# Kernel tuning notes

Measured on AMD Instinct MI355X. Metric: run time of the kernel, lower is better.

Reference implementation:

```python
import jax, jax.numpy as jnp
from jax import lax
import numpy as np

N_LAYERS = 2
HIDDEN = 1024
N_STOCKS = 1024
LB, UB = 0.0, 0.2
REBAL_ITERS = 32  # fixed upper bound; loop converges in 1-2 iters in practice


def setup_inputs() -> dict:
    key = jax.random.key(0)
    ks = jax.random.split(key, 20)
    B, T = 512, 128
    inp = {"x": jax.random.normal(ks[0], (B, T, N_STOCKS), dtype=jnp.float32)}
    k = 1
    for l in range(N_LAYERS):
        in_dim = N_STOCKS if l == 0 else HIDDEN
        s = 1.0 / np.sqrt(HIDDEN)
        inp[f"w_ih_{l}"] = jax.random.uniform(ks[k], (3 * HIDDEN, in_dim), minval=-s, maxval=s); k += 1
        inp[f"w_hh_{l}"] = jax.random.uniform(ks[k], (3 * HIDDEN, HIDDEN), minval=-s, maxval=s); k += 1
        inp[f"b_ih_{l}"] = jax.random.uniform(ks[k], (3 * HIDDEN,), minval=-s, maxval=s); k += 1
        inp[f"b_hh_{l}"] = jax.random.uniform(ks[k], (3 * HIDDEN,), minval=-s, maxval=s); k += 1
    s = 1.0 / np.sqrt(HIDDEN)
    inp["fc_w"] = jax.random.uniform(ks[k], (N_STOCKS, HIDDEN), minval=-s, maxval=s); k += 1
    inp["fc_b"] = jax.random.uniform(ks[k], (N_STOCKS,), minval=-s, maxval=s)
    return inp


def _gru_layer(x, w_ih, w_hh, b_ih, b_hh):
    # x: [B,T,D] -> hidden sequence [B,T,H]; PyTorch GRU cell math
    B, T, _ = x.shape
    H = w_hh.shape[1]
    x_proj = jnp.einsum('btd,gd->btg', x, w_ih) + b_ih  # [B,T,3H]

    def step(h, xp):
        hp = h @ w_hh.T + b_hh
        xr, xz, xn = jnp.split(xp, 3, axis=-1)
        hr, hz, hn = jnp.split(hp, 3, axis=-1)
        r = jax.nn.sigmoid(xr + hr)
        z = jax.nn.sigmoid(xz + hz)
        n = jnp.tanh(xn + r * hn)
        h_new = (1.0 - z) * n + z * h
        return h_new, h_new

    h0 = jnp.zeros((B, H), x.dtype)
    _, hs = lax.scan(step, h0, jnp.swapaxes(x_proj, 0, 1))  # [T,B,H]
    return jnp.swapaxes(hs, 0, 1)


def _rebalance(w, lb, ub, n_iters=REBAL_ITERS):
    # Batched version of the iterative capped-simplex redistribution loop.
    old = w
    wc = jnp.clip(w, lb, ub)
    done = jnp.zeros((w.shape[0],), dtype=bool)

    def body(state, _):
        old, wc, done = state
        leftover = jnp.sum(old - wc, axis=-1, keepdims=True)            # [B,1]
        mask = wc != ub                                                  # nominees
        num = jnp.sum(mask, axis=-1)                                     # [B]
        nom_sum = jnp.sum(jnp.where(mask, wc, 0.0), axis=-1, keepdims=True)
        gift = leftover * wc / jnp.where(nom_sum == 0.0, 1.0, nom_sum)
        wc_new = jnp.where(mask, wc + gift, wc)
        no_nom = num == 0
        over = jnp.any(wc_new > ub, axis=-1)
        new_done = done | no_nom | (~over)
        wc_next = jnp.where(no_nom[:, None], wc,
                            jnp.where(over[:, None], jnp.clip(wc_new, lb, ub), wc_new))
        old_next = jnp.where(no_nom[:, None], old, wc_new)
        wc_out = jnp.where(done[:, None], wc, wc_next)
        old_out = jnp.where(done[:, None], old, old_next)
        return (old_out, wc_out, new_done), None

    (_, wc, _), _ = lax.scan(body, (old, wc, done), None, length=n_iters)
    return wc


def reference(x, w_ih_0, w_hh_0, b_ih_0, b_hh_0, w_ih_1, w_hh_1, b_ih_1, b_hh_1, fc_w, fc_b):
    h = _gru_layer(x, w_ih_0, w_hh_0, b_ih_0, b_hh_0)
    h = _gru_layer(h, w_ih_1, w_hh_1, b_ih_1, b_hh_1)
    h_t = h[:, -1, :]                                   # last time step [B,H]
    logit = h_t @ fc_w.T + fc_b                         # dropout is identity in eval
    logit = jax.nn.silu(logit)
    probs = jax.nn.softmax(logit, axis=-1)
    return _rebalance(probs, LB, UB)
```

## Files before the change

### kernel.cpp

```cpp
#include <hip/hip_runtime.h>
#include <hip/hip_bf16.h>
#include <stdint.h>

#define BB 512
#define TT 128
#define DD 1024
#define HH 1024
#define G3 3072
#define TC 16
#define NCH (TT/TC)
#define NRING 17

typedef __bf16 bft;
typedef __bf16 bf16x8 __attribute__((ext_vector_type(8)));
typedef float f32x4 __attribute__((ext_vector_type(4)));

__device__ __forceinline__ void gl_lds16(const bft* g, void* lds_base_uniform) {
  __builtin_amdgcn_global_load_lds(
      (const __attribute__((address_space(1))) void*)g,
      (__attribute__((address_space(3))) void*)lds_base_uniform,
      16, 0, 0);
}

__device__ __forceinline__ void st_wt_bf16(bft* p, float v) {
  bft h = (bft)v;
  union { bft h; unsigned short u; } cv; cv.h = h;
  unsigned int uv = cv.u;
  asm volatile("global_store_short %0, %1, off sc0 sc1" :: "v"(p), "v"(uv) : "memory");
}
__device__ __forceinline__ void st_wt_f32(float* p, float v) {
  asm volatile("global_store_dword %0, %1, off sc0 sc1" :: "v"(p), "v"(v) : "memory");
}
__device__ __forceinline__ void st_wt_u32(int* p, int v) {
  asm volatile("global_store_dword %0, %1, off sc0 sc1" :: "v"(p), "v"(v) : "memory");
}
__device__ __forceinline__ int ld_co_u32(const int* p) {
  int v;
  asm volatile("global_load_dword %0, %1, off sc0 sc1\n\ts_waitcnt vmcnt(0)"
               : "=v"(v) : "v"(p) : "memory");
  return v;
}

__global__ void k_cvt(const float* __restrict__ in, bft* __restrict__ out, long n) {
  long i = ((long)blockIdx.x * blockDim.x + threadIdx.x) * 8;
  long stride = (long)gridDim.x * blockDim.x * 8;
  for (; i < n; i += stride) {
    float4 a = *(const float4*)(in + i);
    float4 b = *(const float4*)(in + i + 4);
    bf16x8 r;
    r[0] = (bft)a.x; r[1] = (bft)a.y; r[2] = (bft)a.z; r[3] = (bft)a.w;
    r[4] = (bft)b.x; r[5] = (bft)b.y; r[6] = (bft)b.z; r[7] = (bft)b.w;
    *(bf16x8*)(out + i) = r;
  }
}

__global__ void k_gather(const float* __restrict__ x, bft* __restrict__ xc, int t0) {
  long idx = (long)blockIdx.x * blockDim.x + threadIdx.x;
  long elem = idx * 8;
  if (elem >= (long)BB * TC * DD) return;
  long m = elem >> 10;
  int d = (int)(elem & 1023);
  long b = m >> 4; int tc = (int)(m & 15);
  const float* src = x + ((b * TT) + t0 + tc) * (long)DD + d;
  float4 a = *(const float4*)(src);
  float4 c2 = *(const float4*)(src + 4);
  bf16x8 r;
  r[0] = (bft)a.x; r[1] = (bft)a.y; r[2] = (bft)a.z; r[3] = (bft)a.w;
  r[4] = (bft)c2.x; r[5] = (bft)c2.y; r[6] = (bft)c2.z; r[7] = (bft)c2.w;
  *(bf16x8*)(xc + elem) = r;
}

template<int AMODE, int EPI>
__launch_bounds__(256)
__global__ void k_gemm(const bft* __restrict__ A, long lda,
                       const bft* __restrict__ W, long ldw,
                       const float* __restrict__ bias,
                       void* __restrict__ Cout, long ldc,
                       int t0, int K) {
  __shared__ unsigned char sm[32768];
  const int tid  = threadIdx.x;
  const int lane = tid & 63;
  const int wid  = tid >> 6;
  const int m0 = blockIdx.y * 128;
  const int n0 = blockIdx.x * 128;
  const int wm = wid >> 1, wn = wid & 1;

  f32x4 acc[4][4] = {};

  for (int k0 = 0; k0 < K; k0 += 64) {
#pragma unroll
    for (int s = 0; s < 4; ++s) {
      int seg = wid * 4 + s;
      int row = seg * 8 + (lane >> 3);
      int cbs = ((lane & 7) * 16) ^ ((row & 7) << 4);
      int mr = m0 + row;
      long grow = (AMODE == 0) ? (long)mr
                               : (long)(t0 + (mr & (TC - 1))) * BB + (mr >> 4);
      gl_lds16(A + grow * lda + k0 + (cbs >> 1), sm + seg * 1024);
    }
#pragma unroll
    for (int s = 0; s < 4; ++s) {
      int seg = wid * 4 + s;
      int row = seg * 8 + (lane >> 3);
      int cbs = ((lane & 7) * 16) ^ ((row & 7) << 4);
      gl_lds16(W + (long)(n0 + row) * ldw + k0 + (cbs >> 1), sm + 16384 + seg * 1024);
    }
    __syncthreads();
#pragma unroll
    for (int ks = 0; ks < 2; ++ks) {
      int kb = ks * 64 + (lane >> 4) * 16;
      bf16x8 aF[4], bF[4];
#pragma unroll
      for (int mi = 0; mi < 4; ++mi) {
        int row = wm * 64 + mi * 16 + (lane & 15);
        aF[mi] = *(const bf16x8*)(sm + row * 128 + (kb ^ ((row & 7) << 4)));
      }
#pragma unroll
      for (int ni = 0; ni < 4; ++ni) {
        int row = wn * 64 + ni * 16 + (lane & 15);
        bF[ni] = *(const bf16x8*)(sm + 16384 + row * 128 + (kb ^ ((row & 7) << 4)));
      }
#pragma unroll
      for (int mi = 0; mi < 4; ++mi)
#pragma unroll
        for (int ni = 0; ni < 4; ++ni)
          acc[mi][ni] = __builtin_amdgcn_mfma_f32_16x16x32_bf16(aF[mi], bF[ni], acc[mi][ni], 0, 0, 0);
    }
    __syncthreads();
  }

#pragma unroll
  for (int mi = 0; mi < 4; ++mi)
#pragma unroll
    for (int ni = 0; ni < 4; ++ni) {
      int col = n0 + wn * 64 + ni * 16 + (lane & 15);
      float bv = bias[col];
#pragma unroll
      for (int r = 0; r < 4; ++r) {
        long row = m0 + wm * 64 + mi * 16 + (lane >> 4) * 4 + r;
        float v = acc[mi][ni][r] + bv;
        if (EPI == 0) {
          ((bft*)Cout)[row * ldc + col] = (bft)v;
        } else {
          ((float*)Cout)[row * ldc + col] = v / (1.f + expf(-v));
        }
      }
    }
}

template<int L>
__launch_bounds__(256, 1)
__global__ void k_persist(const bft* __restrict__ whh, const float* __restrict__ bhh,
                          const bft* __restrict__ xp,
                          bft* __restrict__ hseq,
                          bft* __restrict__ hseq2,
                          const bft* __restrict__ hzero,
                          float* __restrict__ hfc, int* __restrict__ flags,
                          int t0, int pbase) {
  __shared__ unsigned char sm[163840];
  unsigned char* smW = sm;
  unsigned char* smA = sm + 98304;

  const int tid  = threadIdx.x;
  const int lane = tid & 63;
  const int wid  = tid >> 6;
  const int bid  = blockIdx.x;
  const int xcd = bid & 7, loc = bid >> 3;
  const int mt = xcd >> 1;
  const int nt = (xcd & 1) * 32 + loc;
  const int j0 = nt * 16;
  const int m0 = mt * 128;
  const int j  = j0 + (lane & 15);
  int* gflags = flags + mt * 64;

#pragma unroll
  for (int s8 = 0; s8 < 24; ++s8) {
    int s = wid * 24 + s8;
    int row = s >> 1;
    int half = s & 1;
    int hb = half * 1024 + lane * 16;
    int sb = hb ^ ((row & 7) << 4);
    long grow = (long)(row >> 4) * 1024 + j0 + (row & 15);
    gl_lds16(whh + grow * 1024 + (sb >> 1), smW + s * 1024);
  }
  asm volatile("s_waitcnt vmcnt(0)" ::: "memory");
  __builtin_amdgcn_s_barrier();

  const float br = bhh[j], bz = bhh[1024 + j], bn = bhh[2048 + j];

  auto stageA = [&](const bft* base, int k0, int bufsel) {
    unsigned char* dst = smA + bufsel * 16384;
#pragma unroll
    for (int si = 0; si < 4; ++si) {
      int seg = wid * 4 + si;
      int row = seg * 8 + (lane >> 3);
      int cb = ((lane & 7) * 16) ^ ((row & 7) << 4);
      gl_lds16(base + (long)(m0 + row) * DD + k0 + (cb >> 1), dst + seg * 1024);
    }
  };

  float xg[3][2][4];
  float hp[2][4];

  auto prefXG = [&](int s) {
#pragma unroll
    for (int mi = 0; mi < 2; ++mi)
#pragma unroll
      for (int r = 0; r < 4; ++r) {
        long b = m0 + wid * 32 + mi * 16 + (lane >> 4) * 4 + r;
        long xrow = (b * TC + s) * (long)G3 + j;
        xg[0][mi][r] = (float)xp[xrow];
        xg[1][mi][r] = (float)xp[xrow + 1024];
        xg[2][mi][r] = (float)xp[xrow + 2048];
      }
  };

  prefXG(0);
  if (t0 == 0) {
#pragma unroll
    for (int mi = 0; mi < 2; ++mi)
#pragma unroll
      for (int r = 0; r < 4; ++r) hp[mi][r] = 0.f;
  } else {
#pragma unroll
    for (int mi = 0; mi < 2; ++mi)
#pragma unroll
      for (int r = 0; r < 4; ++r) {
        long b = m0 + wid * 32 + mi * 16 + (lane >> 4) * 4 + r;
        hp[mi][r] = hfc[b * HH + j];
      }
  }
  __builtin_amdgcn_sched_barrier(0);

  for (int s = 0; s < TC; ++s) {
    const int t = t0 + s;

    if (s) {
      int target = pbase + s;
      if (tid < 64) {
        const int* fp = gflags + tid;
        while (ld_co_u32(fp) < target) __builtin_amdgcn_s_sleep(2);
      }
      __syncthreads();
    }

    const bft* Ab;
    if (L == 0) Ab = (t == 0) ? hzero : hseq  + (long)(t - 1) * (BB * (long)DD);
    else        Ab = (t == 0) ? hzero : hseq2 + (long)((t - 1) % NRING) * (BB * (long)DD);

    stageA(Ab, 0, 0);
    stageA(Ab, 64, 1);
    stageA(Ab, 128, 2);

    f32x4 acc[3][2] = {};
#pragma unroll
    for (int k = 0; k < 16; ++k) {
      __builtin_amdgcn_s_barrier();
      if (k < 13) stageA(Ab, (k + 3) * 64, (k + 3) & 3);
      if (k < 13)       asm volatile("s_waitcnt vmcnt(12)" ::: "memory");
      else if (k == 13) asm volatile("s_waitcnt vmcnt(8)" ::: "memory");
      else if (k == 14) asm volatile("s_waitcnt vmcnt(4)" ::: "memory");
      else              asm volatile("s_waitcnt vmcnt(0)" ::: "memory");
      __builtin_amdgcn_s_barrier();
      __builtin_amdgcn_sched_barrier(0);
      const unsigned char* Abuf = smA + (k & 3) * 16384;
#pragma unroll
      for (int ks = 0; ks < 2; ++ks) {
        int kb = ks * 64 + (lane >> 4) * 16;
        bf16x8 aF[2], bF[3];
#pragma unroll
        for (int mi = 0; mi < 2; ++mi) {
          int row = wid * 32 + mi * 16 + (lane & 15);
          aF[mi] = *(const bf16x8*)(Abuf + row * 128 + (kb ^ ((row & 7) << 4)));
        }
#pragma unroll
        for (int g = 0; g < 3; ++g) {
          int wrow = g * 16 + (lane & 15);
          bF[g] = *(const bf16x8*)(smW + wrow * 2048 + ((k * 128 + kb) ^ ((wrow & 7) << 4)));
        }
#pragma unroll
        for (int g = 0; g < 3; ++g)
#pragma unroll
          for (int mi = 0; mi < 2; ++mi)
            acc[g][mi] = __builtin_amdgcn_mfma_f32_16x16x32_bf16(aF[mi], bF[g], acc[g][mi], 0, 0, 0);
      }
    }

    bft* outp = (L == 0) ? hseq  + (long)t * (BB * (long)DD)
                         : hseq2 + (long)(t % NRING) * (BB * (long)DD);
#pragma unroll
    for (int mi = 0; mi < 2; ++mi)
#pragma unroll
      for (int r = 0; r < 4; ++r) {
        long b = m0 + wid * 32 + mi * 16 + (lane >> 4) * 4 + r;
        float hr = acc[0][mi][r] + br;
        float hz = acc[1][mi][r] + bz;
        float hn = acc[2][mi][r] + bn;
        float rg = 1.f / (1.f + expf(-(xg[0][mi][r] + hr)));
        float zg = 1.f / (1.f + expf(-(xg[1][mi][r] + hz)));
        float ng = tanhf(xg[2][mi][r] + rg * hn);
        float hv = (1.f - zg) * ng + zg * hp[mi][r];
        hp[mi][r] = hv;
        st_wt_bf16(outp + b * DD + j, hv);
        if (s == TC - 1) st_wt_f32(hfc + b * HH + j, hv);
      }

    __syncthreads();
    if (s < TC - 1) {
      if (tid == 0) st_wt_u32(gflags + nt, pbase + s + 1);
      prefXG(s + 1);
      __builtin_amdgcn_sched_barrier(0);
    }
  }
}

__device__ __forceinline__ float blk_sum(float v, float* red, int tid) {
#pragma unroll
  for (int o = 32; o; o >>= 1) v += __shfl_xor(v, o);
  if ((tid & 63) == 0) red[tid >> 6] = v;
  __syncthreads();
  v = red[0] + red[1] + red[2] + red[3];
  __syncthreads();
  return v;
}
__device__ __forceinline__ float blk_max(float v, float* red, int tid) {
#pragma unroll
  for (int o = 32; o; o >>= 1) v = fmaxf(v, __shfl_xor(v, o));
  if ((tid & 63) == 0) red[tid >> 6] = v;
  __syncthreads();
  v = fmaxf(fmaxf(red[0], red[1]), fmaxf(red[2], red[3]));
  __syncthreads();
  return v;
}

__launch_bounds__(256)
__global__ void k_smrebal(const float* __restrict__ logits, float* __restrict__ out) {
  __shared__ float red[4];
  const int tid = threadIdx.x;
  const long row = blockIdx.x;
  const float ub = 0.2f, lb = 0.0f;
  float4 lv = *(const float4*)(logits + row * 1024 + tid * 4);

  float m = fmaxf(fmaxf(lv.x, lv.y), fmaxf(lv.z, lv.w));
  m = blk_max(m, red, tid);
  float e[4] = {expf(lv.x - m), expf(lv.y - m), expf(lv.z - m), expf(lv.w - m)};
  float S = blk_sum(e[0] + e[1] + e[2] + e[3], red, tid);

  float old_[4], wc[4];
#pragma unroll
  for (int k = 0; k < 4; ++k) {
    float p = e[k] / S;
    old_[k] = p;
    wc[k] = fminf(fmaxf(p, lb), ub);
  }
  bool done = false;
  for (int it = 0; it < 32 && !done; ++it) {
    float d3 = 0.f, cnt = 0.f, nsum = 0.f;
#pragma unroll
    for (int k = 0; k < 4; ++k) {
      d3 += old_[k] - wc[k];
      bool mk = (wc[k] != ub);
      cnt += mk ? 1.f : 0.f;
      nsum += mk ? wc[k] : 0.f;
    }
    float leftover = blk_sum(d3, red, tid);
    float num = blk_sum(cnt, red, tid);
    float nom_sum = blk_sum(nsum, red, tid);
    float denom = (nom_sum == 0.f) ? 1.f : nom_sum;
    float wcn[4], mx = -1e30f;
#pragma unroll
    for (int k = 0; k < 4; ++k) {
      bool mk = (wc[k] != ub);
      wcn[k] = mk ? wc[k] + leftover * wc[k] / denom : wc[k];
      mx = fmaxf(mx, wcn[k]);
    }
    float gmx = blk_max(mx, red, tid);
    bool no_nom = (num == 0.f);
    bool over = (gmx > ub);
#pragma unroll
    for (int k = 0; k < 4; ++k) {
      float nxt = no_nom ? wc[k] : (over ? fminf(fmaxf(wcn[k], lb), ub) : wcn[k]);
      float oldn = no_nom ? old_[k] : wcn[k];
      wc[k] = nxt;
      old_[k] = oldn;
    }
    done = no_nom || !over;
  }
#pragma unroll
  for (int k = 0; k < 4; ++k) out[row * 1024 + tid * 4 + k] = wc[k];
}

extern "C" void kernel_launch(void* const* d_in, const int* in_sizes, int n_in,
                              void* d_out, int out_size, void* d_ws, size_t ws_size,
                              hipStream_t stream) {
  const float* x      = (const float*)d_in[0];
  const float* wih[2] = {(const float*)d_in[1], (const float*)d_in[5]};
  const float* whh[2] = {(const float*)d_in[2], (const float*)d_in[6]};
  const float* bih[2] = {(const float*)d_in[3], (const float*)d_in[7]};
  const float* bhh[2] = {(const float*)d_in[4], (const float*)d_in[8]};
  const float* fcw    = (const float*)d_in[9];
  const float* fcb    = (const float*)d_in[10];
  float* outp = (float*)d_out;

  unsigned char* ws = (unsigned char*)d_ws;
  size_t off = 0;
  auto alloc = [&](size_t bytes) -> void* {
    void* p = ws + off;
    off += (bytes + 255) & ~(size_t)255;
    return p;
  };
  bft* xchunk  = (bft*)alloc((size_t)BB * TC * DD * 2);
  bft* wihb0   = (bft*)alloc((size_t)G3 * DD * 2);
  bft* whhb0   = (bft*)alloc((size_t)G3 * HH * 2);
  bft* wihb1   = (bft*)alloc((size_t)G3 * HH * 2);
  bft* whhb1   = (bft*)alloc((size_t)G3 * HH * 2);
  bft* fcwb    = (bft*)alloc((size_t)1024 * 1024 * 2);
  bft* xp      = (bft*)alloc((size_t)BB * TC * G3 * 2);
  bft* hseq    = (bft*)alloc((size_t)TT * BB * DD * 2);
  bft* hseq2   = (bft*)alloc((size_t)NRING * BB * DD * 2);
  bft* hzero   = (bft*)alloc((size_t)BB * DD * 2);
  float* hfc   = (float*)alloc((size_t)BB * HH * 4);
  int* flags   = (int*)alloc(1024);
  float* logits= (float*)alloc((size_t)BB * 1024 * 4);
  if (off > ws_size) return;

  bft* wihb[2] = {wihb0, wihb1};
  bft* whhb[2] = {whhb0, whhb1};

  hipMemsetAsync(flags, 0, 1024, stream);
  hipMemsetAsync(hzero, 0, (size_t)BB * DD * 2, stream);

  k_cvt<<<dim3(1536), dim3(256), 0, stream>>>(wih[0], wihb[0], (long)G3 * DD);
  k_cvt<<<dim3(1536), dim3(256), 0, stream>>>(whh[0], whhb[0], (long)G3 * HH);
  k_cvt<<<dim3(1536), dim3(256), 0, stream>>>(wih[1], wihb[1], (long)G3 * HH);
  k_cvt<<<dim3(1536), dim3(256), 0, stream>>>(whh[1], whhb[1], (long)G3 * HH);
  k_cvt<<<dim3(512),  dim3(256), 0, stream>>>(fcw, fcwb, (long)1024 * 1024);

  for (int l = 0; l < 2; ++l) {
    for (int c = 0; c < NCH; ++c) {
      int t0 = c * TC;
      int pbase = (l * NCH + c) * TC;
      if (l == 0) {
        k_gather<<<dim3(4096), dim3(256), 0, stream>>>(x, xchunk, t0);
        k_gemm<0, 0><<<dim3(G3 / 128, (BB * TC) / 128), 256, 0, stream>>>(
            xchunk, DD, wihb[0], DD, bih[0], xp, G3, t0, DD);
        k_persist<0><<<dim3(256), dim3(256), 0, stream>>>(
            whhb[0], bhh[0], xp, hseq, hseq2, hzero, hfc, flags, t0, pbase);
      } else {
        k_gemm<2, 0><<<dim3(G3 / 128, (BB * TC) / 128), 256, 0, stream>>>(
            hseq, DD, wihb[1], DD, bih[1], xp, G3, t0, DD);
        k_persist<1><<<dim3(256), dim3(256), 0, stream>>>(
            whhb[1], bhh[1], xp, hseq, hseq2, hzero, hfc, flags, t0, pbase);
      }
    }
  }
  const bft* hfin = hseq2 + (size_t)((TT - 1) % NRING) * BB * DD;
  k_gemm<0, 1><<<dim3(1024 / 128, BB / 128), 256, 0, stream>>>(
      hfin, DD, fcwb, HH, fcb, logits, 1024, 0, HH);
  k_smrebal<<<dim3(BB), 256, 0, stream>>>(logits, outp);
}
```

Before: 2.993 ms.

## Interleave GRU layers per chunk with ring buffers and fuse fp32 gather into GEMM

Processes both GRU layers chunk by chunk, alternating layer 0 and layer 1, so each layer's hidden states live only in a small ring buffer instead of a full-sequence buffer. The chunk size goes from 16 to 32, which halves the number of launches. The separate gather/convert kernel is removed: the input-projection GEMM now reads fp32 x directly and converts it to bf16 while staging into LDS, instead of using async direct-to-LDS loads. Together these cut launch count and memory traffic. The cost is that fp32 loads are staged synchronously through registers, the ring-slot indexing is more complex, and the xp buffer is larger.

```diff
diff --git a/kernel.cpp b/kernel.cpp
--- a/kernel.cpp
+++ b/kernel.cpp
@@ -7,9 +7,9 @@
 #define DD 1024
 #define HH 1024
 #define G3 3072
-#define TC 16
+#define TC 32
 #define NCH (TT/TC)
-#define NRING 17
+#define NRING 33
 
 typedef __bf16 bft;
 typedef __bf16 bf16x8 __attribute__((ext_vector_type(8)));
@@ -54,25 +54,9 @@
   }
 }
 
-__global__ void k_gather(const float* __restrict__ x, bft* __restrict__ xc, int t0) {
-  long idx = (long)blockIdx.x * blockDim.x + threadIdx.x;
-  long elem = idx * 8;
-  if (elem >= (long)BB * TC * DD) return;
-  long m = elem >> 10;
-  int d = (int)(elem & 1023);
-  long b = m >> 4; int tc = (int)(m & 15);
-  const float* src = x + ((b * TT) + t0 + tc) * (long)DD + d;
-  float4 a = *(const float4*)(src);
-  float4 c2 = *(const float4*)(src + 4);
-  bf16x8 r;
-  r[0] = (bft)a.x; r[1] = (bft)a.y; r[2] = (bft)a.z; r[3] = (bft)a.w;
-  r[4] = (bft)c2.x; r[5] = (bft)c2.y; r[6] = (bft)c2.z; r[7] = (bft)c2.w;
-  *(bf16x8*)(xc + elem) = r;
-}
-
 template<int AMODE, int EPI>
 __launch_bounds__(256)
-__global__ void k_gemm(const bft* __restrict__ A, long lda,
+__global__ void k_gemm(const void* __restrict__ Ap, long lda,
                        const bft* __restrict__ W, long ldw,
                        const float* __restrict__ bias,
                        void* __restrict__ Cout, long ldc,
@@ -88,15 +72,37 @@
   f32x4 acc[4][4] = {};
 
   for (int k0 = 0; k0 < K; k0 += 64) {
-#pragma unroll
-    for (int s = 0; s < 4; ++s) {
-      int seg = wid * 4 + s;
-      int row = seg * 8 + (lane >> 3);
-      int cbs = ((lane & 7) * 16) ^ ((row & 7) << 4);
-      int mr = m0 + row;
-      long grow = (AMODE == 0) ? (long)mr
-                               : (long)(t0 + (mr & (TC - 1))) * BB + (mr >> 4);
-      gl_lds16(A + grow * lda + k0 + (cbs >> 1), sm + seg * 1024);
+    if (AMODE == 1) {
+      const float* Af = (const float*)Ap;
+#pragma unroll
+      for (int s = 0; s < 4; ++s) {
+        int seg = wid * 4 + s;
+        int row = seg * 8 + (lane >> 3);
+        int mr = m0 + row;
+        long grow = (long)(mr >> 5) * TT + t0 + (mr & 31);
+        const float* src = Af + grow * lda + k0 + (lane & 7) * 8;
+        float4 a  = *(const float4*)src;
+        float4 b2 = *(const float4*)(src + 4);
+        bf16x8 r;
+        r[0] = (bft)a.x;  r[1] = (bft)a.y;  r[2] = (bft)a.z;  r[3] = (bft)a.w;
+        r[4] = (bft)b2.x; r[5] = (bft)b2.y; r[6] = (bft)b2.z; r[7] = (bft)b2.w;
+        *(bf16x8*)(sm + seg * 1024 + (lane >> 3) * 128 +
+                   (((lane & 7) * 16) ^ ((row & 7) << 4))) = r;
+      }
+    } else {
+      const bft* Ab = (const bft*)Ap;
+#pragma unroll
+      for (int s = 0; s < 4; ++s) {
+        int seg = wid * 4 + s;
+        int row = seg * 8 + (lane >> 3);
+        int cbs = ((lane & 7) * 16) ^ ((row & 7) << 4);
+        int mr = m0 + row;
+        long grow;
+        if (AMODE == 0) grow = mr;
+        else { int sl = t0 + (mr & 31); if (sl >= NRING) sl -= NRING;
+               grow = (long)sl * BB + (mr >> 5); }
+        gl_lds16(Ab + grow * lda + k0 + (cbs >> 1), sm + seg * 1024);
+      }
     }
 #pragma unroll
     for (int s = 0; s < 4; ++s) {
@@ -148,15 +154,12 @@
     }
 }
 
-template<int L>
 __launch_bounds__(256, 1)
 __global__ void k_persist(const bft* __restrict__ whh, const float* __restrict__ bhh,
                           const bft* __restrict__ xp,
-                          bft* __restrict__ hseq,
-                          bft* __restrict__ hseq2,
-                          const bft* __restrict__ hzero,
+                          bft* __restrict__ ring,
                           float* __restrict__ hfc, int* __restrict__ flags,
-                          int t0, int pbase) {
+                          int t0s, int first, int pbase) {
   __shared__ unsigned char sm[163840];
   unsigned char* smW = sm;
   unsigned char* smA = sm + 98304;
@@ -216,7 +219,7 @@
   };
 
   prefXG(0);
-  if (t0 == 0) {
+  if (first) {
 #pragma unroll
     for (int mi = 0; mi < 2; ++mi)
 #pragma unroll
@@ -233,8 +236,6 @@
   __builtin_amdgcn_sched_barrier(0);
 
   for (int s = 0; s < TC; ++s) {
-    const int t = t0 + s;
-
     if (s) {
       int target = pbase + s;
       if (tid < 64) {
@@ -244,50 +245,50 @@
       __syncthreads();
     }
 
-    const bft* Ab;
-    if (L == 0) Ab = (t == 0) ? hzero : hseq  + (long)(t - 1) * (BB * (long)DD);
-    else        Ab = (t == 0) ? hzero : hseq2 + (long)((t - 1) % NRING) * (BB * (long)DD);
-
-    stageA(Ab, 0, 0);
-    stageA(Ab, 64, 1);
-    stageA(Ab, 128, 2);
+    int sl = t0s + s; if (sl >= NRING) sl -= NRING;
+    int psl = sl ? sl - 1 : NRING - 1;
 
     f32x4 acc[3][2] = {};
-#pragma unroll
-    for (int k = 0; k < 16; ++k) {
-      __builtin_amdgcn_s_barrier();
-      if (k < 13) stageA(Ab, (k + 3) * 64, (k + 3) & 3);
-      if (k < 13)       asm volatile("s_waitcnt vmcnt(12)" ::: "memory");
-      else if (k == 13) asm volatile("s_waitcnt vmcnt(8)" ::: "memory");
-      else if (k == 14) asm volatile("s_waitcnt vmcnt(4)" ::: "memory");
-      else              asm volatile("s_waitcnt vmcnt(0)" ::: "memory");
-      __builtin_amdgcn_s_barrier();
-      __builtin_amdgcn_sched_barrier(0);
-      const unsigned char* Abuf = smA + (k & 3) * 16384;
-#pragma unroll
-      for (int ks = 0; ks < 2; ++ks) {
-        int kb = ks * 64 + (lane >> 4) * 16;
-        bf16x8 aF[2], bF[3];
-#pragma unroll
-        for (int mi = 0; mi < 2; ++mi) {
-          int row = wid * 32 + mi * 16 + (lane & 15);
-          aF[mi] = *(const bf16x8*)(Abuf + row * 128 + (kb ^ ((row & 7) << 4)));
+    if (!(first && s == 0)) {
+      const bft* Ab = ring + (long)psl * (BB * (long)DD);
+      stageA(Ab, 0, 0);
+      stageA(Ab, 64, 1);
+      stageA(Ab, 128, 2);
+#pragma unroll
+      for (int k = 0; k < 16; ++k) {
+        __builtin_amdgcn_s_barrier();
+        if (k < 13) stageA(Ab, (k + 3) * 64, (k + 3) & 3);
+        if (k < 13)       asm volatile("s_waitcnt vmcnt(12)" ::: "memory");
+        else if (k == 13) asm volatile("s_waitcnt vmcnt(8)" ::: "memory");
+        else if (k == 14) asm volatile("s_waitcnt vmcnt(4)" ::: "memory");
+        else              asm volatile("s_waitcnt vmcnt(0)" ::: "memory");
+        __builtin_amdgcn_s_barrier();
+        __builtin_amdgcn_sched_barrier(0);
+        const unsigned char* Abuf = smA + (k & 3) * 16384;
+#pragma unroll
+        for (int ks = 0; ks < 2; ++ks) {
+          int kb = ks * 64 + (lane >> 4) * 16;
+          bf16x8 aF[2], bF[3];
+#pragma unroll
+          for (int mi = 0; mi < 2; ++mi) {
+            int row = wid * 32 + mi * 16 + (lane & 15);
+            aF[mi] = *(const bf16x8*)(Abuf + row * 128 + (kb ^ ((row & 7) << 4)));
+          }
+#pragma unroll
+          for (int g = 0; g < 3; ++g) {
+            int wrow = g * 16 + (lane & 15);
+            bF[g] = *(const bf16x8*)(smW + wrow * 2048 + ((k * 128 + kb) ^ ((wrow & 7) << 4)));
+          }
+#pragma unroll
+          for (int g = 0; g < 3; ++g)
+#pragma unroll
+            for (int mi = 0; mi < 2; ++mi)
+              acc[g][mi] = __builtin_amdgcn_mfma_f32_16x16x32_bf16(aF[mi], bF[g], acc[g][mi], 0, 0, 0);
         }
-#pragma unroll
-        for (int g = 0; g < 3; ++g) {
-          int wrow = g * 16 + (lane & 15);
-          bF[g] = *(const bf16x8*)(smW + wrow * 2048 + ((k * 128 + kb) ^ ((wrow & 7) << 4)));
-        }
-#pragma unroll
-        for (int g = 0; g < 3; ++g)
-#pragma unroll
-          for (int mi = 0; mi < 2; ++mi)
-            acc[g][mi] = __builtin_amdgcn_mfma_f32_16x16x32_bf16(aF[mi], bF[g], acc[g][mi], 0, 0, 0);
-      }
-    }
-
-    bft* outp = (L == 0) ? hseq  + (long)t * (BB * (long)DD)
-                         : hseq2 + (long)(t % NRING) * (BB * (long)DD);
+      }
+    }
+
+    bft* outp = ring + (long)sl * (BB * (long)DD);
 #pragma unroll
     for (int mi = 0; mi < 2; ++mi)
 #pragma unroll
@@ -409,52 +410,42 @@
     off += (bytes + 255) & ~(size_t)255;
     return p;
   };
-  bft* xchunk  = (bft*)alloc((size_t)BB * TC * DD * 2);
   bft* wihb0   = (bft*)alloc((size_t)G3 * DD * 2);
   bft* whhb0   = (bft*)alloc((size_t)G3 * HH * 2);
   bft* wihb1   = (bft*)alloc((size_t)G3 * HH * 2);
   bft* whhb1   = (bft*)alloc((size_t)G3 * HH * 2);
   bft* fcwb    = (bft*)alloc((size_t)1024 * 1024 * 2);
   bft* xp      = (bft*)alloc((size_t)BB * TC * G3 * 2);
-  bft* hseq    = (bft*)alloc((size_t)TT * BB * DD * 2);
-  bft* hseq2   = (bft*)alloc((size_t)NRING * BB * DD * 2);
-  bft* hzero   = (bft*)alloc((size_t)BB * DD * 2);
-  float* hfc   = (float*)alloc((size_t)BB * HH * 4);
+  bft* ring0   = (bft*)alloc((size_t)NRING * BB * DD * 2);
+  bft* ring1   = (bft*)alloc((size_t)NRING * BB * DD * 2);
+  float* hfc0  = (float*)alloc((size_t)BB * HH * 4);
+  float* hfc1  = (float*)alloc((size_t)BB * HH * 4);
   int* flags   = (int*)alloc(1024);
   float* logits= (float*)alloc((size_t)BB * 1024 * 4);
   if (off > ws_size) return;
 
-  bft* wihb[2] = {wihb0, wihb1};
-  bft* whhb[2] = {whhb0, whhb1};
-
   hipMemsetAsync(flags, 0, 1024, stream);
-  hipMemsetAsync(hzero, 0, (size_t)BB * DD * 2, stream);
-
-  k_cvt<<<dim3(1536), dim3(256), 0, stream>>>(wih[0], wihb[0], (long)G3 * DD);
-  k_cvt<<<dim3(1536), dim3(256), 0, stream>>>(whh[0], whhb[0], (long)G3 * HH);
-  k_cvt<<<dim3(1536), dim3(256), 0, stream>>>(wih[1], wihb[1], (long)G3 * HH);
-  k_cvt<<<dim3(1536), dim3(256), 0, stream>>>(whh[1], whhb[1], (long)G3 * HH);
+
+  k_cvt<<<dim3(1536), dim3(256), 0, stream>>>(wih[0], wihb0, (long)G3 * DD);
+  k_cvt<<<dim3(1536), dim3(256), 0, stream>>>(whh[0], whhb0, (long)G3 * HH);
+  k_cvt<<<dim3(1536), dim3(256), 0, stream>>>(wih[1], wihb1, (long)G3 * HH);
+  k_cvt<<<dim3(1536), dim3(256), 0, stream>>>(whh[1], whhb1, (long)G3 * HH);
   k_cvt<<<dim3(512),  dim3(256), 0, stream>>>(fcw, fcwb, (long)1024 * 1024);
 
-  for (int l = 0; l < 2; ++l) {
-    for (int c = 0; c < NCH; ++c) {
-      int t0 = c * TC;
-      int pbase = (l * NCH + c) * TC;
-      if (l == 0) {
-        k_gather<<<dim3(4096), dim3(256), 0, stream>>>(x, xchunk, t0);
-        k_gemm<0, 0><<<dim3(G3 / 128, (BB * TC) / 128), 256, 0, stream>>>(
-            xchunk, DD, wihb[0], DD, bih[0], xp, G3, t0, DD);
-        k_persist<0><<<dim3(256), dim3(256), 0, stream>>>(
-            whhb[0], bhh[0], xp, hseq, hseq2, hzero, hfc, flags, t0, pbase);
-      } else {
-        k_gemm<2, 0><<<dim3(G3 / 128, (BB * TC) / 128), 256, 0, stream>>>(
-            hseq, DD, wihb[1], DD, bih[1], xp, G3, t0, DD);
-        k_persist<1><<<dim3(256), dim3(256), 0, stream>>>(
-            whhb[1], bhh[1], xp, hseq, hseq2, hzero, hfc, flags, t0, pbase);
-      }
-    }
-  }
-  const bft* hfin = hseq2 + (size_t)((TT - 1) % NRING) * BB * DD;
+  for (int c = 0; c < NCH; ++c) {
+    int t0 = c * TC;
+    int t0s = t0 % NRING;
+    int first = (c == 0) ? 1 : 0;
+    k_gemm<1, 0><<<dim3(G3 / 128, (BB * TC) / 128), 256, 0, stream>>>(
+        x, DD, wihb0, DD, bih[0], xp, G3, t0, DD);
+    k_persist<<<dim3(256), dim3(256), 0, stream>>>(
+        whhb0, bhh[0], xp, ring0, hfc0, flags, t0s, first, (2 * c) * TC);
+    k_gemm<2, 0><<<dim3(G3 / 128, (BB * TC) / 128), 256, 0, stream>>>(
+        ring0, DD, wihb1, DD, bih[1], xp, G3, t0s, DD);
+    k_persist<<<dim3(256), dim3(256), 0, stream>>>(
+        whhb1, bhh[1], xp, ring1, hfc1, flags, t0s, first, (2 * c + 1) * TC);
+  }
+  const bft* hfin = ring1 + (size_t)((TT - 1) % NRING) * BB * DD;
   k_gemm<0, 1><<<dim3(1024 / 128, BB / 128), 256, 0, stream>>>(
       hfin, DD, fcwb, HH, fcb, logits, 1024, 0, HH);
   k_smrebal<<<dim3(BB), 256, 0, stream>>>(logits, outp);
```

Result: slower. 3.081 ms (+2.9%).
